# Kernel optimization log

Measured on AMD Instinct MI355X. Metric: run time of the kernel, lower is better.

The kernel has to match this reference:

```python
import jax, jax.numpy as jnp
import numpy as np

HIDDEN = 64

def setup_inputs() -> dict:
    key = jax.random.key(0)
    ks = jax.random.split(key, 10)
    B, E = 8, 200000
    h = jax.random.normal(ks[0], (B, E, HIDDEN), dtype=jnp.float32)
    J = jax.random.normal(ks[1], (B, E, 1), dtype=jnp.float32)
    b_in = jax.random.normal(ks[2], (B, E, 1), dtype=jnp.float32)
    b_out = jax.random.normal(ks[3], (B, E, 1), dtype=jnp.float32)
    d_in = HIDDEN + 4
    # PyTorch Linear default init: U(-1/sqrt(fan_in), 1/sqrt(fan_in))
    def lin(kw, kb, fan_in, fan_out):
        bound = 1.0 / np.sqrt(fan_in)
        W = jax.random.uniform(kw, (fan_in, fan_out), minval=-bound, maxval=bound, dtype=jnp.float32)
        b = jax.random.uniform(kb, (fan_out,), minval=-bound, maxval=bound, dtype=jnp.float32)
        return W, b
    W1, b1 = lin(ks[4], ks[5], d_in, 64)
    W2, b2 = lin(ks[6], ks[7], 64, 64)
    W3, b3 = lin(ks[8], ks[9], 64, 5)
    return {"h": h, "J": J, "b_in": b_in, "b_out": b_out,
            "W1": W1, "b1": b1, "W2": W2, "b2": b2, "W3": W3, "b3": b3}

def reference(h, J, b_in, b_out, W1, b1, W2, b2, W3, b3):
    # concat order matches torch.cat((h, b_in, b_out, J, -J), 2)
    x = jnp.concatenate((h, b_in, b_out, J, -J), axis=2)  # [B,E,hidden+4]
    x = jax.nn.relu(jnp.einsum('bei,io->beo', x, W1) + b1)
    x = jax.nn.relu(jnp.einsum('bei,io->beo', x, W2) + b2)
    message = jnp.einsum('bei,io->beo', x, W3) + b3  # [B,E,5]
    return message
```

## Files before the change

### kernel.cpp

```cpp
#include <hip/hip_runtime.h>

typedef __bf16 bf16x8 __attribute__((ext_vector_type(8)));
typedef float  f32x4  __attribute__((ext_vector_type(4)));

#define MFMA(A, B, C) __builtin_amdgcn_mfma_f32_16x16x32_bf16((A), (B), (C), 0, 0, 0)

__global__ __launch_bounds__(256, 2)
void msg_mlp(const float* __restrict__ hbuf, const float* __restrict__ Jbuf,
             const float* __restrict__ binb, const float* __restrict__ boutb,
             const float* __restrict__ W1, const float* __restrict__ b1,
             const float* __restrict__ W2, const float* __restrict__ b2,
             const float* __restrict__ W3, const float* __restrict__ b3,
             float* __restrict__ out, int n_rows, int n_pairs)
{
    const int lane = threadIdx.x & 63;
    const int e = lane & 15;
    const int q = lane >> 4;
    const int wid = blockIdx.x * (blockDim.x >> 6) + (threadIdx.x >> 6);
    const int nw  = gridDim.x * (blockDim.x >> 6);

    bf16x8 a1[4][2];
#pragma unroll
    for (int mt = 0; mt < 4; ++mt)
#pragma unroll
      for (int kk = 0; kk < 2; ++kk)
#pragma unroll
        for (int i = 0; i < 8; ++i)
          a1[mt][kk][i] = (__bf16)W1[(16*q + 8*kk + i)*64 + 16*mt + e];

    bf16x8 a1x[4];
#pragma unroll
    for (int mt = 0; mt < 4; ++mt) {
      const int o = 16*mt + e;
      float w0;
      if      (q == 0) w0 =  W1[64*64 + o];
      else if (q == 1) w0 =  W1[65*64 + o];
      else if (q == 2) w0 =  W1[66*64 + o];
      else             w0 = -W1[67*64 + o];
      a1x[mt][0] = (__bf16)w0;
      a1x[mt][1] = (q == 0) ? (__bf16)b1[o] : (__bf16)0.0f;
#pragma unroll
      for (int i = 2; i < 8; ++i) a1x[mt][i] = (__bf16)0.0f;
    }

    bf16x8 a2[4][2];
#pragma unroll
    for (int mt = 0; mt < 4; ++mt)
#pragma unroll
      for (int kk = 0; kk < 2; ++kk)
#pragma unroll
        for (int i = 0; i < 8; ++i) {
          const int f = 16*(2*kk + (i>>2)) + 4*q + (i&3);
          a2[mt][kk][i] = (__bf16)W2[f*64 + 16*mt + e];
        }
    bf16x8 a3[2];
#pragma unroll
    for (int kk = 0; kk < 2; ++kk)
#pragma unroll
      for (int i = 0; i < 8; ++i) {
        const int f = 16*(2*kk + (i>>2)) + 4*q + (i&3);
        a3[kk][i] = (e < 5) ? (__bf16)W3[f*5 + e] : (__bf16)0.0f;
      }
    float b2r[4][4];
#pragma unroll
    for (int mt = 0; mt < 4; ++mt)
#pragma unroll
      for (int r = 0; r < 4; ++r) b2r[mt][r] = b2[16*mt + 4*q + r];
    float b3r[4];
#pragma unroll
    for (int r = 0; r < 4; ++r) b3r[r] = (4*q + r < 5) ? b3[4*q + r] : 0.0f;

    const float* sptr = (q == 0) ? binb : (q == 1) ? boutb : Jbuf;
    const __bf16 biasf = (q == 0) ? (__bf16)1.0f : (__bf16)0.0f;

    auto issue = [&](int tt, f32x4& h0, f32x4& h1, f32x4& h2, f32x4& h3, float& s) {
      int re = tt * 16 + e;
      if (re >= n_rows) re = n_rows - 1;
      const float* hr = hbuf + (size_t)re * 64 + q * 16;
      h0 = *(const f32x4*)(hr);
      h1 = *(const f32x4*)(hr + 4);
      h2 = *(const f32x4*)(hr + 8);
      h3 = *(const f32x4*)(hr + 12);
      s = sptr[re];
    };

    auto compute_store = [&](f32x4 h0, f32x4 h1, f32x4 h2, f32x4 h3, float s, int tt) {
      bf16x8 xb0, xb1, xb2;
#pragma unroll
      for (int i = 0; i < 4; ++i) {
        xb0[i]     = (__bf16)h0[i];
        xb0[i + 4] = (__bf16)h1[i];
        xb1[i]     = (__bf16)h2[i];
        xb1[i + 4] = (__bf16)h3[i];
      }
      xb2[0] = (__bf16)s; xb2[1] = biasf;
#pragma unroll
      for (int i = 2; i < 8; ++i) xb2[i] = (__bf16)0.0f;

      f32x4 acc1[4];
#pragma unroll
      for (int mt = 0; mt < 4; ++mt) {
        acc1[mt] = (f32x4){0.f, 0.f, 0.f, 0.f};
        acc1[mt] = MFMA(a1[mt][0], xb0, acc1[mt]);
        acc1[mt] = MFMA(a1[mt][1], xb1, acc1[mt]);
        acc1[mt] = MFMA(a1x[mt],   xb2, acc1[mt]);
      }
      bf16x8 y[2];
#pragma unroll
      for (int kk = 0; kk < 2; ++kk)
#pragma unroll
        for (int i = 0; i < 8; ++i)
          y[kk][i] = (__bf16)fmaxf(acc1[2*kk + (i>>2)][i & 3], 0.0f);

      f32x4 acc2[4];
#pragma unroll
      for (int mt = 0; mt < 4; ++mt) {
        acc2[mt] = (f32x4){b2r[mt][0], b2r[mt][1], b2r[mt][2], b2r[mt][3]};
        acc2[mt] = MFMA(a2[mt][0], y[0], acc2[mt]);
        acc2[mt] = MFMA(a2[mt][1], y[1], acc2[mt]);
      }
      bf16x8 z[2];
#pragma unroll
      for (int kk = 0; kk < 2; ++kk)
#pragma unroll
        for (int i = 0; i < 8; ++i)
          z[kk][i] = (__bf16)fmaxf(acc2[2*kk + (i>>2)][i & 3], 0.0f);

      f32x4 acc3 = (f32x4){b3r[0], b3r[1], b3r[2], b3r[3]};
      acc3 = MFMA(a3[0], z[0], acc3);
      acc3 = MFMA(a3[1], z[1], acc3);

      const int rowi = tt * 16 + e;
      if (rowi < n_rows) {
        float* orow = out + (size_t)rowi * 5;
        if (q == 0) {
          orow[0] = acc3[0]; orow[1] = acc3[1];
          orow[2] = acc3[2]; orow[3] = acc3[3];
        } else if (q == 1) {
          orow[4] = acc3[0];
        }
      }
    };

    int p = wid;
    f32x4 c00, c01, c02, c03, c10, c11, c12, c13;
    float s0 = 0.f, s1 = 0.f;
    if (p < n_pairs) {
      issue(2*p,     c00, c01, c02, c03, s0);
      issue(2*p + 1, c10, c11, c12, c13, s1);
    }

    for (; p < n_pairs; p += nw) {
      f32x4 n00, n01, n02, n03, n10, n11, n12, n13;
      float t0 = 0.f, t1 = 0.f;
      const int pn = p + nw;
      if (pn < n_pairs) {
        issue(2*pn,     n00, n01, n02, n03, t0);
        issue(2*pn + 1, n10, n11, n12, n13, t1);
      }

      compute_store(c00, c01, c02, c03, s0, 2*p);
      compute_store(c10, c11, c12, c13, s1, 2*p + 1);

      c00 = n00; c01 = n01; c02 = n02; c03 = n03; s0 = t0;
      c10 = n10; c11 = n11; c12 = n12; c13 = n13; s1 = t1;
    }
}

extern "C" void kernel_launch(void* const* d_in, const int* in_sizes, int n_in,
                              void* d_out, int out_size, void* d_ws, size_t ws_size,
                              hipStream_t stream) {
    const float* h     = (const float*)d_in[0];
    const float* J     = (const float*)d_in[1];
    const float* b_in  = (const float*)d_in[2];
    const float* b_out = (const float*)d_in[3];
    const float* W1    = (const float*)d_in[4];
    const float* b1    = (const float*)d_in[5];
    const float* W2    = (const float*)d_in[6];
    const float* b2    = (const float*)d_in[7];
    const float* W3    = (const float*)d_in[8];
    const float* b3    = (const float*)d_in[9];
    float* out = (float*)d_out;

    const int n_rows  = in_sizes[1];
    const int n_pairs = (n_rows + 31) / 32;

    dim3 grid(512), block(256);
    hipLaunchKernelGGL(msg_mlp, grid, block, 0, stream,
                       h, J, b_in, b_out, W1, b1, W2, b2, W3, b3,
                       out, n_rows, n_pairs);
}
```

Measured before the change: 103.1 us.

## Stage h tiles through LDS with direct global-to-LDS loads, double-buffered

Replaces the register prefetch of two 16-row tiles with global_load_lds transfers of one 16-row tile into a per-wave double-buffered LDS region. The LDS layout is XOR-swizzled so the MFMA operand reads avoid bank conflicts, and a manual vmcnt wait plus a sched_barrier order the pipeline. The goal is to free registers and make the dominant 51 MB h stream more efficient. The trade-offs are a 32 KB LDS footprint per block and less work per loop iteration. The waitcnt depends on the compiler's instruction order, and the tail clamp reloads the current tile rather than bounds-checking the last partial tile.

Result: faster. 96.90 us (-6.0%).

```diff
diff --git a/kernel.cpp b/kernel.cpp
--- a/kernel.cpp
+++ b/kernel.cpp
@@ -3,7 +3,11 @@
 typedef __bf16 bf16x8 __attribute__((ext_vector_type(8)));
 typedef float  f32x4  __attribute__((ext_vector_type(4)));
 
+typedef const void GV __attribute__((address_space(1)));
+typedef void       LV __attribute__((address_space(3)));
+
 #define MFMA(A, B, C) __builtin_amdgcn_mfma_f32_16x16x32_bf16((A), (B), (C), 0, 0, 0)
+#define GLL(gp, lp) __builtin_amdgcn_global_load_lds((GV*)(gp), (LV*)(lp), 16, 0, 0)
 
 __global__ __launch_bounds__(256, 2)
 void msg_mlp(const float* __restrict__ hbuf, const float* __restrict__ Jbuf,
@@ -11,13 +15,24 @@
              const float* __restrict__ W1, const float* __restrict__ b1,
              const float* __restrict__ W2, const float* __restrict__ b2,
              const float* __restrict__ W3, const float* __restrict__ b3,
-             float* __restrict__ out, int n_rows, int n_pairs)
+             float* __restrict__ out, int n_rows, int n_tiles)
 {
+    __shared__ __align__(16) char smem[32768];
     const int lane = threadIdx.x & 63;
     const int e = lane & 15;
     const int q = lane >> 4;
-    const int wid = blockIdx.x * (blockDim.x >> 6) + (threadIdx.x >> 6);
-    const int nw  = gridDim.x * (blockDim.x >> 6);
+    const int wv = (int)(threadIdx.x >> 6);
+    const int wid = blockIdx.x * 4 + wv;
+    const int nw  = gridDim.x * 4;
+    char* wbase = smem + wv * 8192;
+
+    const int o_e = 16 * (lane ^ q);
+    const int o_o = 16 * (lane ^ (q + 4));
+    const int X   = (e & 7) << 4;
+    const int d0 = 256*e + ((64*q +  0) ^ X);
+    const int d1 = 256*e + ((64*q + 16) ^ X);
+    const int d2 = 256*e + ((64*q + 32) ^ X);
+    const int d3 = 256*e + ((64*q + 48) ^ X);
 
     bf16x8 a1[4][2];
 #pragma unroll
@@ -73,27 +88,42 @@
     const float* sptr = (q == 0) ? binb : (q == 1) ? boutb : Jbuf;
     const __bf16 biasf = (q == 0) ? (__bf16)1.0f : (__bf16)0.0f;
 
-    auto issue = [&](int tt, f32x4& h0, f32x4& h1, f32x4& h2, f32x4& h3, float& s) {
-      int re = tt * 16 + e;
-      if (re >= n_rows) re = n_rows - 1;
-      const float* hr = hbuf + (size_t)re * 64 + q * 16;
-      h0 = *(const f32x4*)(hr);
-      h1 = *(const f32x4*)(hr + 4);
-      h2 = *(const f32x4*)(hr + 8);
-      h3 = *(const f32x4*)(hr + 12);
-      s = sptr[re];
+    auto stage = [&](int tt, char* dst) {
+      const char* g = (const char*)hbuf + (size_t)tt * 4096;
+      GLL(g +        o_e, dst);
+      GLL(g + 1024 + o_o, dst + 1024);
+      GLL(g + 2048 + o_e, dst + 2048);
+      GLL(g + 3072 + o_o, dst + 3072);
     };
 
-    auto compute_store = [&](f32x4 h0, f32x4 h1, f32x4 h2, f32x4 h3, float s, int tt) {
+    int t = wid;
+    if (t >= n_tiles) return;
+    stage(t, wbase);
+    float scur = sptr[(size_t)t * 16 + e];
+    int cur = 0;
+
+    for (; t < n_tiles; t += nw) {
+      int tn = t + nw; if (tn >= n_tiles) tn = t;
+      stage(tn, wbase + ((cur ^ 1) << 12));
+      float snext = sptr[(size_t)tn * 16 + e];
+
+      asm volatile("s_waitcnt vmcnt(5)" ::: "memory");
+
+      const char* src = wbase + (cur << 12);
+      const f32x4 v0 = *(const f32x4*)(src + d0);
+      const f32x4 v1 = *(const f32x4*)(src + d1);
+      const f32x4 v2 = *(const f32x4*)(src + d2);
+      const f32x4 v3 = *(const f32x4*)(src + d3);
+
       bf16x8 xb0, xb1, xb2;
 #pragma unroll
       for (int i = 0; i < 4; ++i) {
-        xb0[i]     = (__bf16)h0[i];
-        xb0[i + 4] = (__bf16)h1[i];
-        xb1[i]     = (__bf16)h2[i];
-        xb1[i + 4] = (__bf16)h3[i];
-      }
-      xb2[0] = (__bf16)s; xb2[1] = biasf;
+        xb0[i]     = (__bf16)v0[i];
+        xb0[i + 4] = (__bf16)v1[i];
+        xb1[i]     = (__bf16)v2[i];
+        xb1[i + 4] = (__bf16)v3[i];
+      }
+      xb2[0] = (__bf16)scur; xb2[1] = biasf;
 #pragma unroll
       for (int i = 2; i < 8; ++i) xb2[i] = (__bf16)0.0f;
 
@@ -130,7 +160,7 @@
       acc3 = MFMA(a3[0], z[0], acc3);
       acc3 = MFMA(a3[1], z[1], acc3);
 
-      const int rowi = tt * 16 + e;
+      const int rowi = t * 16 + e;
       if (rowi < n_rows) {
         float* orow = out + (size_t)rowi * 5;
         if (q == 0) {
@@ -140,30 +170,10 @@
           orow[4] = acc3[0];
         }
       }
-    };
-
-    int p = wid;
-    f32x4 c00, c01, c02, c03, c10, c11, c12, c13;
-    float s0 = 0.f, s1 = 0.f;
-    if (p < n_pairs) {
-      issue(2*p,     c00, c01, c02, c03, s0);
-      issue(2*p + 1, c10, c11, c12, c13, s1);
-    }
-
-    for (; p < n_pairs; p += nw) {
-      f32x4 n00, n01, n02, n03, n10, n11, n12, n13;
-      float t0 = 0.f, t1 = 0.f;
-      const int pn = p + nw;
-      if (pn < n_pairs) {
-        issue(2*pn,     n00, n01, n02, n03, t0);
-        issue(2*pn + 1, n10, n11, n12, n13, t1);
-      }
-
-      compute_store(c00, c01, c02, c03, s0, 2*p);
-      compute_store(c10, c11, c12, c13, s1, 2*p + 1);
-
-      c00 = n00; c01 = n01; c02 = n02; c03 = n03; s0 = t0;
-      c10 = n10; c11 = n11; c12 = n12; c13 = n13; s1 = t1;
+      __builtin_amdgcn_sched_barrier(0);
+
+      scur = snext;
+      cur ^= 1;
     }
 }
 
@@ -183,10 +193,10 @@
     float* out = (float*)d_out;
 
     const int n_rows  = in_sizes[1];
-    const int n_pairs = (n_rows + 31) / 32;
+    const int n_tiles = (n_rows + 15) / 16;
 
     dim3 grid(512), block(256);
     hipLaunchKernelGGL(msg_mlp, grid, block, 0, stream,
                        h, J, b_in, b_out, W1, b1, W2, b2, W3, b3,
-                       out, n_rows, n_pairs);
+                       out, n_rows, n_tiles);
 }
```
